# Performance work log

Hardware: AMD Instinct MI355X
Metric: run time of the kernel (lower is better)

The kernel has to match this reference:

```python
import jax, jax.numpy as jnp
import numpy as np

N_NODES = 50000
N_EDGES = 800000
IN_DIM, HID_DIM, OUT_DIM = 128, 256, 64


def setup_inputs() -> dict:
    key = jax.random.key(0)
    k1, k2, k3, k4 = jax.random.split(key, 4)
    x = jax.random.normal(k1, (N_NODES, IN_DIM), dtype=jnp.float32)
    edge_index = jax.random.randint(k2, (2, N_EDGES), 0, N_NODES, dtype=jnp.int32)
    # Glorot-ish scaled weights
    W1 = jax.random.normal(k3, (IN_DIM, HID_DIM), dtype=jnp.float32) * (1.0 / np.sqrt(IN_DIM))
    W2 = jax.random.normal(k4, (HID_DIM, OUT_DIM), dtype=jnp.float32) * (1.0 / np.sqrt(HID_DIM))
    b1 = jnp.zeros((HID_DIM,), dtype=jnp.float32)
    b2 = jnp.zeros((OUT_DIM,), dtype=jnp.float32)
    return {"x": x, "edge_index": edge_index, "W1": W1, "b1": b1, "W2": W2, "b2": b2}


def _gcn_conv(x, src, dst, deg_inv_sqrt, W, b):
    # transform first (PyG GCNConv order), then edge-normalized scatter-add
    h = x @ W                                        # [N, D_out]
    norm = deg_inv_sqrt[src] * deg_inv_sqrt[dst]     # [E]
    msgs = h[src] * norm[:, None]                    # [E, D_out]
    agg = jax.ops.segment_sum(msgs, dst, num_segments=x.shape[0])
    return agg + b


def reference(x, edge_index, W1, b1, W2, b2):
    n = x.shape[0]
    loops = jnp.arange(n, dtype=edge_index.dtype)
    src = jnp.concatenate([edge_index[0], loops])    # add self-loops
    dst = jnp.concatenate([edge_index[1], loops])
    deg = jax.ops.segment_sum(jnp.ones_like(dst, dtype=x.dtype), dst, num_segments=n)
    deg_inv_sqrt = jnp.where(deg > 0, jax.lax.rsqrt(jnp.maximum(deg, 1e-12)), 0.0)
    h = jax.nn.relu(_gcn_conv(x, src, dst, deg_inv_sqrt, W1, b1))
    h = _gcn_conv(h, src, dst, deg_inv_sqrt, W2, b2)
    return jax.nn.log_softmax(h, axis=1)
```

## Files before the change

kernel.cpp:

```cpp
#include <hip/hip_runtime.h>
#include <hip/hip_bf16.h>
#include <math.h>

#define N_NODES 50000
#define N_EDGES 800000
#define IN_DIM 128
#define HID_DIM 256
#define OUT_DIM 64
#define NPART 196
#define CAP 8192
#define CHUNK 2048
#define NPB ((N_EDGES + CHUNK - 1) / CHUNK)

typedef __attribute__((ext_vector_type(8))) short bf16x8;
typedef __attribute__((ext_vector_type(4))) short short4v;
typedef __attribute__((ext_vector_type(4))) float f32x4;

__device__ inline short f2bf(float f) {
    unsigned u = __float_as_uint(f);
    unsigned r = (u + 0x7fffu + ((u >> 16) & 1u)) >> 16;
    return (short)r;
}
__device__ inline float bf_lo(unsigned u) { return __uint_as_float(u << 16); }
__device__ inline float bf_hi(unsigned u) { return __uint_as_float(u & 0xffff0000u); }

__global__ __launch_bounds__(256) void part1_pack_kernel(const int* __restrict__ src,
                                                         const int* __restrict__ dst,
                                                         int* __restrict__ coarseCursor,
                                                         uint2* __restrict__ sedge,
                                                         const float* __restrict__ W1,
                                                         const float* __restrict__ W2,
                                                         short* __restrict__ Bp1,
                                                         short* __restrict__ Bp2, int E) {
    __shared__ int cnt_l[NPART];
    __shared__ int pref[NPART];
    __shared__ int gbase[NPART];
    __shared__ int ws4[4];
    __shared__ uint2 stage[CHUNK];
    int tid = threadIdx.x;
    if (blockIdx.x >= NPB) {
        int idx = (blockIdx.x - NPB) * 256 + tid;
        const float* W; short* Bp; int N;
        const int T1 = (IN_DIM / 32) * (HID_DIM / 16) * 64;
        const int T2 = (HID_DIM / 32) * (OUT_DIM / 16) * 64;
        if (idx < T1) { W = W1; Bp = Bp1; N = HID_DIM; }
        else { idx -= T1; if (idx >= T2) return; W = W2; Bp = Bp2; N = OUT_DIM; }
        int lane = idx & 63;
        int frag = idx >> 6;
        int ntiles = N >> 4;
        int nt = frag % ntiles;
        int kt = frag / ntiles;
        int col = nt * 16 + (lane & 15);
        int krow = kt * 32 + (lane >> 4) * 8;
        bf16x8 pk;
        #pragma unroll
        for (int j = 0; j < 8; j++) pk[j] = f2bf(W[(size_t)(krow + j) * N + col]);
        *((bf16x8*)(Bp + (size_t)idx * 8)) = pk;
        return;
    }
    int e0 = blockIdx.x * CHUNK;
    if (tid < NPART) cnt_l[tid] = 0;
    __syncthreads();
    int es[CHUNK / 256], ed[CHUNK / 256];
    #pragma unroll
    for (int j = 0; j < CHUNK / 256; j++) {
        int e = e0 + j * 256 + tid;
        if (e < E) {
            es[j] = src[e]; ed[j] = dst[e];
            atomicAdd(&cnt_l[ed[j] >> 8], 1);
        } else ed[j] = -1;
    }
    __syncthreads();
    int lane = tid & 63, wid = tid >> 6;
    int v = (tid < NPART) ? cnt_l[tid] : 0;
    int s = v;
    #pragma unroll
    for (int off = 1; off < 64; off <<= 1) {
        int t = __shfl_up(s, off, 64);
        if (lane >= off) s += t;
    }
    if (lane == 63) ws4[wid] = s;
    __syncthreads();
    int wp = 0;
    #pragma unroll
    for (int w = 0; w < 4; w++) wp += (w < wid) ? ws4[w] : 0;
    int excl = s - v + wp;
    if (tid < NPART) pref[tid] = excl;
    __syncthreads();
    if (tid < NPART) cnt_l[tid] = excl;
    __syncthreads();
    #pragma unroll
    for (int j = 0; j < CHUNK / 256; j++) {
        if (ed[j] >= 0) {
            int c = ed[j] >> 8;
            int p = atomicAdd(&cnt_l[c], 1);
            stage[p] = make_uint2((unsigned)es[j], (unsigned)ed[j]);
        }
    }
    __syncthreads();
    if (tid < NPART) {
        int cl = cnt_l[tid] - pref[tid];
        gbase[tid] = (cl > 0) ? (tid * CAP + atomicAdd(&coarseCursor[tid], cl)) : 0;
    }
    __syncthreads();
    int total = (e0 + CHUNK <= E) ? CHUNK : (E - e0);
    for (int i = tid; i < total; i += 256) {
        uint2 ev = stage[i];
        int c = (int)(ev.y >> 8);
        sedge[gbase[c] + (i - pref[c])] = ev;
    }
}

__global__ __launch_bounds__(256) void part2_kernel(const uint2* __restrict__ sedge,
                                                    const int* __restrict__ coarseCnt,
                                                    int* __restrict__ offs,
                                                    int* __restrict__ cntg,
                                                    float* __restrict__ dis,
                                                    int* __restrict__ ssrc,
                                                    const float* __restrict__ x,
                                                    short* __restrict__ xb, int n) {
    __shared__ int kcnt[256];
    __shared__ int ws4[4];
    __shared__ float sdis[256];
    int b = blockIdx.x, tid = threadIdx.x;
    int base = b * CAP;
    int cb = coarseCnt[b];
    kcnt[tid] = 0;
    __syncthreads();
    for (int i = tid; i < cb; i += 256) {
        uint2 ev = sedge[base + i];
        atomicAdd(&kcnt[ev.y & 255], 1);
    }
    __syncthreads();
    int v = kcnt[tid];
    int lane = tid & 63, wid = tid >> 6;
    int s = v;
    #pragma unroll
    for (int off = 1; off < 64; off <<= 1) {
        int t = __shfl_up(s, off, 64);
        if (lane >= off) s += t;
    }
    if (lane == 63) ws4[wid] = s;
    __syncthreads();
    int wp = 0;
    #pragma unroll
    for (int w = 0; w < 4; w++) wp += (w < wid) ? ws4[w] : 0;
    int excl = s - v + wp;
    int node = b * 256 + tid;
    float dn = rsqrtf((float)v + 1.0f);
    if (node < n) {
        offs[node] = base + excl;
        cntg[node] = v;
        dis[node] = dn;
    }
    sdis[tid] = dn;
    __syncthreads();
    kcnt[tid] = base + excl;
    __syncthreads();
    for (int i = tid; i < cb; i += 256) {
        uint2 ev = sedge[base + i];
        int pos = atomicAdd(&kcnt[ev.y & 255], 1);
        ssrc[pos] = (int)ev.x;
    }
    int rlane = tid & 31, rgrp = tid >> 5;
    for (int rb = 0; rb < 32; rb++) {
        int row = rb * 8 + rgrp;
        int nd = b * 256 + row;
        if (nd >= n) break;
        float d2 = sdis[row];
        float4 vv = ((const float4*)(x + (size_t)nd * IN_DIM))[rlane];
        short4v o = {f2bf(vv.x * d2), f2bf(vv.y * d2), f2bf(vv.z * d2), f2bf(vv.w * d2)};
        *((short4v*)(xb + (size_t)nd * IN_DIM + rlane * 4)) = o;
    }
}

__global__ __launch_bounds__(256) void agg1_kernel(const short* __restrict__ xb,
                                                   const int* __restrict__ ssrc,
                                                   const int* __restrict__ offs,
                                                   const int* __restrict__ cnt,
                                                   const float* __restrict__ dis,
                                                   short* __restrict__ aggx, int n) {
    int lane = threadIdx.x & 63;
    int node = blockIdx.x * 4 + (threadIdx.x >> 6);
    if (node >= n) return;
    int start = __builtin_amdgcn_readfirstlane(offs[node]);
    int c = __builtin_amdgcn_readfirstlane(cnt[node]);
    const unsigned* base = (const unsigned*)xb;
    float a0 = 0.0f, a1 = 0.0f;
    int j = 0;
    for (; j + 4 <= c; j += 4) {
        int i0 = ssrc[start + j];
        int i1 = ssrc[start + j + 1];
        int i2 = ssrc[start + j + 2];
        int i3 = ssrc[start + j + 3];
        unsigned u0 = base[(size_t)i0 * (IN_DIM / 2) + lane];
        unsigned u1 = base[(size_t)i1 * (IN_DIM / 2) + lane];
        unsigned u2 = base[(size_t)i2 * (IN_DIM / 2) + lane];
        unsigned u3 = base[(size_t)i3 * (IN_DIM / 2) + lane];
        a0 += bf_lo(u0); a1 += bf_hi(u0);
        a0 += bf_lo(u1); a1 += bf_hi(u1);
        a0 += bf_lo(u2); a1 += bf_hi(u2);
        a0 += bf_lo(u3); a1 += bf_hi(u3);
    }
    for (; j < c; j++) {
        int i0 = ssrc[start + j];
        unsigned u0 = base[(size_t)i0 * (IN_DIM / 2) + lane];
        a0 += bf_lo(u0); a1 += bf_hi(u0);
    }
    unsigned us = base[(size_t)node * (IN_DIM / 2) + lane];
    a0 += bf_lo(us); a1 += bf_hi(us);
    float dn = dis[node];
    a0 *= dn; a1 *= dn;
    unsigned o = ((unsigned)(unsigned short)f2bf(a1) << 16) | (unsigned)(unsigned short)f2bf(a0);
    ((unsigned*)aggx)[(size_t)node * (IN_DIM / 2) + lane] = o;
}

#define H1_STRIDE 264
__global__ __launch_bounds__(256) void gemm_fused_kernel(const short* __restrict__ A,
                                                         const short* __restrict__ Bp1,
                                                         const short* __restrict__ Bp2,
                                                         const float* __restrict__ b1,
                                                         const float* __restrict__ dis,
                                                         short* __restrict__ h2, int M) {
    __shared__ short lds_h1[4][16][H1_STRIDE];
    int lane = threadIdx.x & 63;
    int w = threadIdx.x >> 6;
    int rowBase = blockIdx.x * 64 + w * 16;
    int arow = rowBase + (lane & 15);
    int kseg = lane >> 4;
    int col0 = lane & 15;

    constexpr int NT1 = HID_DIM / 16;
    f32x4 acc1[NT1] = {};
    #pragma unroll
    for (int kt = 0; kt < IN_DIM / 32; kt++) {
        bf16x8 a = {};
        if (arow < M)
            a = *((const bf16x8*)(A + (size_t)arow * IN_DIM + kt * 32 + kseg * 8));
        #pragma unroll
        for (int nt = 0; nt < NT1; nt++) {
            bf16x8 b = *((const bf16x8*)(Bp1 + ((size_t)(kt * NT1 + nt) * 64 + lane) * 8));
            acc1[nt] = __builtin_amdgcn_mfma_f32_16x16x32_bf16(a, b, acc1[nt], 0, 0, 0);
        }
    }
    #pragma unroll
    for (int nt = 0; nt < NT1; nt++) {
        float bv = b1[nt * 16 + col0];
        #pragma unroll
        for (int i = 0; i < 4; i++) {
            float v = fmaxf(acc1[nt][i] + bv, 0.0f);
            lds_h1[w][kseg * 4 + i][nt * 16 + col0] = f2bf(v);
        }
    }
    constexpr int NT2 = OUT_DIM / 16;
    f32x4 acc2[NT2] = {};
    #pragma unroll
    for (int kt = 0; kt < HID_DIM / 32; kt++) {
        bf16x8 a = *((const bf16x8*)&lds_h1[w][lane & 15][kt * 32 + kseg * 8]);
        #pragma unroll
        for (int nt = 0; nt < NT2; nt++) {
            bf16x8 b = *((const bf16x8*)(Bp2 + ((size_t)(kt * NT2 + nt) * 64 + lane) * 8));
            acc2[nt] = __builtin_amdgcn_mfma_f32_16x16x32_bf16(a, b, acc2[nt], 0, 0, 0);
        }
    }
    #pragma unroll
    for (int i = 0; i < 4; i++) {
        int r = rowBase + kseg * 4 + i;
        if (r >= M) continue;
        float sc = dis[r];
        #pragma unroll
        for (int nt = 0; nt < NT2; nt++)
            h2[(size_t)r * OUT_DIM + nt * 16 + col0] = f2bf(acc2[nt][i] * sc);
    }
}

__global__ __launch_bounds__(256) void agg2_kernel(const short* __restrict__ h2,
                                                   const int* __restrict__ ssrc,
                                                   const int* __restrict__ offs,
                                                   const int* __restrict__ cnt,
                                                   const float* __restrict__ dis,
                                                   const float* __restrict__ b2,
                                                   float* __restrict__ out, int n) {
    int lane = threadIdx.x & 63;
    int node = blockIdx.x * 4 + (threadIdx.x >> 6);
    if (node >= n) return;
    int start = __builtin_amdgcn_readfirstlane(offs[node]);
    int c = __builtin_amdgcn_readfirstlane(cnt[node]);
    const unsigned short* base = (const unsigned short*)h2;
    float a = 0.0f;
    int j = 0;
    for (; j + 4 <= c; j += 4) {
        int i0 = ssrc[start + j];
        int i1 = ssrc[start + j + 1];
        int i2 = ssrc[start + j + 2];
        int i3 = ssrc[start + j + 3];
        unsigned short u0 = base[(size_t)i0 * OUT_DIM + lane];
        unsigned short u1 = base[(size_t)i1 * OUT_DIM + lane];
        unsigned short u2 = base[(size_t)i2 * OUT_DIM + lane];
        unsigned short u3 = base[(size_t)i3 * OUT_DIM + lane];
        a += __uint_as_float((unsigned)u0 << 16);
        a += __uint_as_float((unsigned)u1 << 16);
        a += __uint_as_float((unsigned)u2 << 16);
        a += __uint_as_float((unsigned)u3 << 16);
    }
    for (; j < c; j++) {
        int i0 = ssrc[start + j];
        unsigned short u0 = base[(size_t)i0 * OUT_DIM + lane];
        a += __uint_as_float((unsigned)u0 << 16);
    }
    unsigned short us = base[(size_t)node * OUT_DIM + lane];
    float dn = dis[node];
    a = (a + __uint_as_float((unsigned)us << 16)) * dn + b2[lane];
    float m = a;
    #pragma unroll
    for (int off = 1; off < 64; off <<= 1) m = fmaxf(m, __shfl_xor(m, off, 64));
    float e = expf(a - m);
    float sum = e;
    #pragma unroll
    for (int off = 1; off < 64; off <<= 1) sum += __shfl_xor(sum, off, 64);
    out[(size_t)node * OUT_DIM + lane] = a - m - logf(sum);
}

extern "C" void kernel_launch(void* const* d_in, const int* in_sizes, int n_in,
                              void* d_out, int out_size, void* d_ws, size_t ws_size,
                              hipStream_t stream) {
    const float* x  = (const float*)d_in[0];
    const int*   ei = (const int*)d_in[1];
    const float* W1 = (const float*)d_in[2];
    const float* b1 = (const float*)d_in[3];
    const float* W2 = (const float*)d_in[4];
    const float* b2 = (const float*)d_in[5];
    float* out = (float*)d_out;
    char* ws = (char*)d_ws;

    const int* srcp = ei;
    const int* dstp = ei + N_EDGES;

    int*   coarseCursor = (int*)(ws);
    int*   offs   = (int*)(ws + 4096);
    int*   cntg   = (int*)(ws + 262144);
    float* dis    = (float*)(ws + 524288);
    short* Bp1    = (short*)(ws + 786432);
    short* Bp2    = (short*)(ws + 851968);
    int*   ssrc   = (int*)(ws + 917504);
    uint2* sedge  = (uint2*)(ws + 7340032);
    short* aggx   = (short*)(ws + 7340032);
    short* xb     = (short*)(ws + 20185088);
    short* h2     = (short*)(ws + 32985088);

    hipMemsetAsync(coarseCursor, 0, NPART * 4, stream);

    part1_pack_kernel<<<NPB + 24, 256, 0, stream>>>(srcp, dstp, coarseCursor, sedge,
                                                    W1, W2, Bp1, Bp2, N_EDGES);
    part2_kernel<<<NPART, 256, 0, stream>>>(sedge, coarseCursor, offs, cntg, dis, ssrc,
                                            x, xb, N_NODES);
    agg1_kernel<<<(N_NODES + 3) / 4, 256, 0, stream>>>(xb, ssrc, offs, cntg, dis, aggx, N_NODES);
    gemm_fused_kernel<<<(N_NODES + 63) / 64, 256, 0, stream>>>(aggx, Bp1, Bp2, b1, dis,
                                                               h2, N_NODES);
    agg2_kernel<<<(N_NODES + 3) / 4, 256, 0, stream>>>(h2, ssrc, offs, cntg, dis, b2, out, N_NODES);
}
```

Baseline: 205.8 us.

## Replace two-level partitioned CSR build with global atomic histogram, scan, scatter

Drops the coarse-partition staging (LDS bucketing into an intermediate sedge buffer followed by a per-partition fine sort). The CSR is now built by a global per-node atomic histogram, a per-block scan into fixed CAP-sized slots, and a scatter pass that claims positions with global atomics. This removes one round trip of intermediate edge storage and the LDS work, but moves all the counting and placement onto contended global atomics. Edge order within each node's list is no longer deterministic, which only affects floating-point summation order.

```diff
diff --git a/kernel.cpp b/kernel.cpp
--- a/kernel.cpp
+++ b/kernel.cpp
@@ -9,8 +9,6 @@
 #define OUT_DIM 64
 #define NPART 196
 #define CAP 8192
-#define CHUNK 2048
-#define NPB ((N_EDGES + CHUNK - 1) / CHUNK)
 
 typedef __attribute__((ext_vector_type(8))) short bf16x8;
 typedef __attribute__((ext_vector_type(4))) short short4v;
@@ -24,27 +22,20 @@
 __device__ inline float bf_lo(unsigned u) { return __uint_as_float(u << 16); }
 __device__ inline float bf_hi(unsigned u) { return __uint_as_float(u & 0xffff0000u); }
 
-__global__ __launch_bounds__(256) void part1_pack_kernel(const int* __restrict__ src,
-                                                         const int* __restrict__ dst,
-                                                         int* __restrict__ coarseCursor,
-                                                         uint2* __restrict__ sedge,
-                                                         const float* __restrict__ W1,
-                                                         const float* __restrict__ W2,
-                                                         short* __restrict__ Bp1,
-                                                         short* __restrict__ Bp2, int E) {
-    __shared__ int cnt_l[NPART];
-    __shared__ int pref[NPART];
-    __shared__ int gbase[NPART];
-    __shared__ int ws4[4];
-    __shared__ uint2 stage[CHUNK];
-    int tid = threadIdx.x;
-    if (blockIdx.x >= NPB) {
-        int idx = (blockIdx.x - NPB) * 256 + tid;
+__global__ __launch_bounds__(256) void hist_pack_kernel(const int* __restrict__ dst,
+                                                        int* __restrict__ cntg,
+                                                        const float* __restrict__ W1,
+                                                        const float* __restrict__ W2,
+                                                        short* __restrict__ Bp1,
+                                                        short* __restrict__ Bp2, int E) {
+    int gtid = blockIdx.x * 256 + threadIdx.x;
+    const int T1 = (IN_DIM / 32) * (HID_DIM / 16) * 64;
+    const int T2 = (HID_DIM / 32) * (OUT_DIM / 16) * 64;
+    if (gtid < T1 + T2) {
+        int idx = gtid;
         const float* W; short* Bp; int N;
-        const int T1 = (IN_DIM / 32) * (HID_DIM / 16) * 64;
-        const int T2 = (HID_DIM / 32) * (OUT_DIM / 16) * 64;
         if (idx < T1) { W = W1; Bp = Bp1; N = HID_DIM; }
-        else { idx -= T1; if (idx >= T2) return; W = W2; Bp = Bp2; N = OUT_DIM; }
+        else { idx -= T1; W = W2; Bp = Bp2; N = OUT_DIM; }
         int lane = idx & 63;
         int frag = idx >> 6;
         int ntiles = N >> 4;
@@ -56,23 +47,24 @@
         #pragma unroll
         for (int j = 0; j < 8; j++) pk[j] = f2bf(W[(size_t)(krow + j) * N + col]);
         *((bf16x8*)(Bp + (size_t)idx * 8)) = pk;
-        return;
-    }
-    int e0 = blockIdx.x * CHUNK;
-    if (tid < NPART) cnt_l[tid] = 0;
-    __syncthreads();
-    int es[CHUNK / 256], ed[CHUNK / 256];
-    #pragma unroll
-    for (int j = 0; j < CHUNK / 256; j++) {
-        int e = e0 + j * 256 + tid;
-        if (e < E) {
-            es[j] = src[e]; ed[j] = dst[e];
-            atomicAdd(&cnt_l[ed[j] >> 8], 1);
-        } else ed[j] = -1;
-    }
-    __syncthreads();
+    }
+    int stride = gridDim.x * 256;
+    for (int e = gtid; e < E; e += stride)
+        atomicAdd(&cntg[dst[e]], 1);
+}
+
+__global__ __launch_bounds__(256) void scan_prep_kernel(const int* __restrict__ cntg,
+                                                        int* __restrict__ offs,
+                                                        int* __restrict__ cursor,
+                                                        float* __restrict__ dis,
+                                                        const float* __restrict__ x,
+                                                        short* __restrict__ xb, int n) {
+    __shared__ int ws4[4];
+    __shared__ float sdis[256];
+    int b = blockIdx.x, tid = threadIdx.x;
+    int nd = b * 256 + tid;
+    int v = (nd < n) ? cntg[nd] : 0;
     int lane = tid & 63, wid = tid >> 6;
-    int v = (tid < NPART) ? cnt_l[tid] : 0;
     int s = v;
     #pragma unroll
     for (int off = 1; off < 64; off <<= 1) {
@@ -85,92 +77,38 @@
     #pragma unroll
     for (int w = 0; w < 4; w++) wp += (w < wid) ? ws4[w] : 0;
     int excl = s - v + wp;
-    if (tid < NPART) pref[tid] = excl;
-    __syncthreads();
-    if (tid < NPART) cnt_l[tid] = excl;
-    __syncthreads();
-    #pragma unroll
-    for (int j = 0; j < CHUNK / 256; j++) {
-        if (ed[j] >= 0) {
-            int c = ed[j] >> 8;
-            int p = atomicAdd(&cnt_l[c], 1);
-            stage[p] = make_uint2((unsigned)es[j], (unsigned)ed[j]);
-        }
-    }
-    __syncthreads();
-    if (tid < NPART) {
-        int cl = cnt_l[tid] - pref[tid];
-        gbase[tid] = (cl > 0) ? (tid * CAP + atomicAdd(&coarseCursor[tid], cl)) : 0;
-    }
-    __syncthreads();
-    int total = (e0 + CHUNK <= E) ? CHUNK : (E - e0);
-    for (int i = tid; i < total; i += 256) {
-        uint2 ev = stage[i];
-        int c = (int)(ev.y >> 8);
-        sedge[gbase[c] + (i - pref[c])] = ev;
-    }
-}
-
-__global__ __launch_bounds__(256) void part2_kernel(const uint2* __restrict__ sedge,
-                                                    const int* __restrict__ coarseCnt,
-                                                    int* __restrict__ offs,
-                                                    int* __restrict__ cntg,
-                                                    float* __restrict__ dis,
-                                                    int* __restrict__ ssrc,
-                                                    const float* __restrict__ x,
-                                                    short* __restrict__ xb, int n) {
-    __shared__ int kcnt[256];
-    __shared__ int ws4[4];
-    __shared__ float sdis[256];
-    int b = blockIdx.x, tid = threadIdx.x;
-    int base = b * CAP;
-    int cb = coarseCnt[b];
-    kcnt[tid] = 0;
-    __syncthreads();
-    for (int i = tid; i < cb; i += 256) {
-        uint2 ev = sedge[base + i];
-        atomicAdd(&kcnt[ev.y & 255], 1);
-    }
-    __syncthreads();
-    int v = kcnt[tid];
-    int lane = tid & 63, wid = tid >> 6;
-    int s = v;
-    #pragma unroll
-    for (int off = 1; off < 64; off <<= 1) {
-        int t = __shfl_up(s, off, 64);
-        if (lane >= off) s += t;
-    }
-    if (lane == 63) ws4[wid] = s;
-    __syncthreads();
-    int wp = 0;
-    #pragma unroll
-    for (int w = 0; w < 4; w++) wp += (w < wid) ? ws4[w] : 0;
-    int excl = s - v + wp;
-    int node = b * 256 + tid;
     float dn = rsqrtf((float)v + 1.0f);
-    if (node < n) {
-        offs[node] = base + excl;
-        cntg[node] = v;
-        dis[node] = dn;
+    if (nd < n) {
+        int o = b * CAP + excl;
+        offs[nd] = o;
+        cursor[nd] = o;
+        dis[nd] = dn;
     }
     sdis[tid] = dn;
     __syncthreads();
-    kcnt[tid] = base + excl;
-    __syncthreads();
-    for (int i = tid; i < cb; i += 256) {
-        uint2 ev = sedge[base + i];
-        int pos = atomicAdd(&kcnt[ev.y & 255], 1);
-        ssrc[pos] = (int)ev.x;
-    }
     int rlane = tid & 31, rgrp = tid >> 5;
     for (int rb = 0; rb < 32; rb++) {
         int row = rb * 8 + rgrp;
-        int nd = b * 256 + row;
-        if (nd >= n) break;
+        int nd2 = b * 256 + row;
+        if (nd2 >= n) break;
         float d2 = sdis[row];
-        float4 vv = ((const float4*)(x + (size_t)nd * IN_DIM))[rlane];
+        float4 vv = ((const float4*)(x + (size_t)nd2 * IN_DIM))[rlane];
         short4v o = {f2bf(vv.x * d2), f2bf(vv.y * d2), f2bf(vv.z * d2), f2bf(vv.w * d2)};
-        *((short4v*)(xb + (size_t)nd * IN_DIM + rlane * 4)) = o;
+        *((short4v*)(xb + (size_t)nd2 * IN_DIM + rlane * 4)) = o;
+    }
+}
+
+__global__ __launch_bounds__(256) void scatter_kernel(const int* __restrict__ src,
+                                                      const int* __restrict__ dst,
+                                                      int* __restrict__ cursor,
+                                                      int* __restrict__ ssrc, int E) {
+    int gtid = blockIdx.x * 256 + threadIdx.x;
+    int stride = gridDim.x * 256;
+    for (int e = gtid; e < E; e += stride) {
+        int d = dst[e];
+        int sv = src[e];
+        int pos = atomicAdd(&cursor[d], 1);
+        ssrc[pos] = sv;
     }
 }
 
@@ -336,24 +274,22 @@
     const int* srcp = ei;
     const int* dstp = ei + N_EDGES;
 
-    int*   coarseCursor = (int*)(ws);
-    int*   offs   = (int*)(ws + 4096);
-    int*   cntg   = (int*)(ws + 262144);
-    float* dis    = (float*)(ws + 524288);
-    short* Bp1    = (short*)(ws + 786432);
-    short* Bp2    = (short*)(ws + 851968);
-    int*   ssrc   = (int*)(ws + 917504);
-    uint2* sedge  = (uint2*)(ws + 7340032);
-    short* aggx   = (short*)(ws + 7340032);
-    short* xb     = (short*)(ws + 20185088);
-    short* h2     = (short*)(ws + 32985088);
-
-    hipMemsetAsync(coarseCursor, 0, NPART * 4, stream);
-
-    part1_pack_kernel<<<NPB + 24, 256, 0, stream>>>(srcp, dstp, coarseCursor, sedge,
-                                                    W1, W2, Bp1, Bp2, N_EDGES);
-    part2_kernel<<<NPART, 256, 0, stream>>>(sedge, coarseCursor, offs, cntg, dis, ssrc,
-                                            x, xb, N_NODES);
+    int*   cntg   = (int*)(ws);
+    int*   offs   = (int*)(ws + 262144);
+    int*   cursor = (int*)(ws + 524288);
+    float* dis    = (float*)(ws + 786432);
+    short* Bp1    = (short*)(ws + 1048576);
+    short* Bp2    = (short*)(ws + 1114112);
+    int*   ssrc   = (int*)(ws + 1146880);
+    short* xb     = (short*)(ws + 7602176);
+    short* aggx   = (short*)(ws + 20447232);
+    short* h2     = (short*)(ws + 33280000);
+
+    hipMemsetAsync(cntg, 0, N_NODES * 4, stream);
+
+    hist_pack_kernel<<<1024, 256, 0, stream>>>(dstp, cntg, W1, W2, Bp1, Bp2, N_EDGES);
+    scan_prep_kernel<<<NPART, 256, 0, stream>>>(cntg, offs, cursor, dis, x, xb, N_NODES);
+    scatter_kernel<<<1024, 256, 0, stream>>>(srcp, dstp, cursor, ssrc, N_EDGES);
     agg1_kernel<<<(N_NODES + 3) / 4, 256, 0, stream>>>(xb, ssrc, offs, cntg, dis, aggx, N_NODES);
     gemm_fused_kernel<<<(N_NODES + 63) / 64, 256, 0, stream>>>(aggx, Bp1, Bp2, b1, dis,
                                                                h2, N_NODES);
```

Measured after the change: 275.9 us. 1.34x slower.
